# Optimization experiments

Hardware: AMD Instinct MI355X
Metric: run time of the kernel (lower is better)

## Reference

```python
import jax, jax.numpy as jnp
import numpy as np

H = 32        # num heads
D = 80        # head dim
HID = 2560    # hidden size = H*D
ROT = 32      # rotary dim = int(0.4*80)
THETA = 10000.0
T = 2048      # total packed tokens
B = 4         # sequences
SEQ = 512     # tokens per sequence
CACHE = 4096  # paged cache slots


def setup_inputs() -> dict:
    key = jax.random.key(0)
    ks = jax.random.split(key, 10)
    bound = 1.0 / np.sqrt(HID)

    def lin(k):
        kw, kb = jax.random.split(k)
        W = jax.random.uniform(kw, (HID, HID), jnp.float32, -bound, bound)
        b = jax.random.uniform(kb, (HID,), jnp.float32, -bound, bound)
        return W, b

    Wq, bq = lin(ks[0])
    Wk, bk = lin(ks[1])
    Wv, bv = lin(ks[2])
    Wd, bd = lin(ks[3])
    h = jax.random.normal(ks[4], (T, HID), jnp.float32)
    return {
        "h": h,
        "k_cache": jnp.zeros((CACHE, HID), jnp.float32),
        "v_cache": jnp.zeros((CACHE, HID), jnp.float32),
        "positions": (jnp.arange(T) % SEQ).astype(jnp.int32),
        "offsets": (jnp.arange(B + 1) * SEQ).astype(jnp.int32),
        "cache_indices": jnp.arange(T, dtype=jnp.int32),
        "Wq": Wq, "bq": bq, "Wk": Wk, "bk": bk,
        "Wv": Wv, "bv": bv, "Wd": Wd, "bd": bd,
    }


def _rotate_half(x):
    x1, x2 = jnp.split(x, 2, axis=-1)
    return jnp.concatenate([-x2, x1], axis=-1)


def reference(h, k_cache, v_cache, positions, offsets, cache_indices,
              Wq, bq, Wk, bk, Wv, bv, Wd, bd):
    # QKV projections (torch Linear: x @ W.T + b)
    q = h @ Wq.T + bq
    k = h @ Wk.T + bk
    v = h @ Wv.T + bv

    q3 = q.reshape(T, H, D)
    k3 = k.reshape(T, H, D)

    # partial RoPE on first ROT dims of each head
    pos = positions.astype(jnp.float32)
    inv_freq = 1.0 / (THETA ** (jnp.arange(0, ROT, 2, dtype=jnp.float32) / ROT))
    freqs = pos[:, None] * inv_freq                      # [T, ROT/2]
    emb = jnp.concatenate([freqs, freqs], axis=-1)       # [T, ROT]
    cos = jnp.cos(emb)[:, None, :]                       # [T, 1, ROT]
    sin = jnp.sin(emb)[:, None, :]

    q_rot, q_pass = q3[..., :ROT], q3[..., ROT:]
    k_rot, k_pass = k3[..., :ROT], k3[..., ROT:]
    q_rot = q_rot * cos + _rotate_half(q_rot) * sin
    k_rot = k_rot * cos + _rotate_half(k_rot) * sin
    q3 = jnp.concatenate([q_rot, q_pass], axis=-1)
    k3 = jnp.concatenate([k_rot, k_pass], axis=-1)

    # prompt_init=True path: scatter rotated k and v into paged caches
    new_k_cache = k_cache.at[cache_indices].set(k3.reshape(T, HID))
    new_v_cache = v_cache.at[cache_indices].set(v)

    # variable-length causal attention over packed sequences
    scale = D ** -0.5
    scores = jnp.einsum('thd,shd->hts', q3, k3) * scale   # [H, T, T]
    idx = jnp.arange(T)
    seg = jnp.searchsorted(offsets[1:], idx, side='right')
    mask = (seg[:, None] == seg[None, :]) & (idx[:, None] >= idx[None, :])
    scores = jnp.where(mask[None], scores, jnp.float32(-1e30))
    p = jax.nn.softmax(scores, axis=-1)
    o = jnp.einsum('hts,shd->thd', p, v.reshape(T, H, D)).reshape(T, HID)

    out = o @ Wd.T + bd
    return out, new_k_cache, new_v_cache
```

## Files before the change

### kernel.cpp

```cpp
#include <hip/hip_runtime.h>
#include <cstdint>
#include <cstddef>


#define HIDDEN 2560
#define SEQT 2048
#define NHEADS 32
#define DHEAD 80
#define NSEG 4
#define SEGLEN 512
#define CACHE_ROWS 4096
#define QSCALE 0.11180339887498949f

typedef __bf16 bf16_8 __attribute__((ext_vector_type(8)));
typedef unsigned short u16x8 __attribute__((ext_vector_type(8)));
typedef float f32x4 __attribute__((ext_vector_type(4)));

__device__ __forceinline__ unsigned short f2bf(float f) {
  unsigned int u = __builtin_bit_cast(unsigned int, f);
  u += 0x7fffu + ((u >> 16) & 1u);
  return (unsigned short)(u >> 16);
}
__device__ __forceinline__ float bf2f(unsigned short s) {
  unsigned int u = ((unsigned int)s) << 16;
  return __builtin_bit_cast(float, u);
}

__device__ __forceinline__ void gload16(const unsigned short* g, unsigned short* l) {
  __builtin_amdgcn_global_load_lds(
      (const __attribute__((address_space(1))) unsigned int*)g,
      (__attribute__((address_space(3))) unsigned int*)l, 16, 0, 0);
}

#define BAR() asm volatile("s_barrier" ::: "memory")
#define LGKM0()                                          \
  do {                                                   \
    asm volatile("s_waitcnt lgkmcnt(0)" ::: "memory");   \
    __builtin_amdgcn_sched_barrier(0);                   \
  } while (0)
#define PRIO(x) __builtin_amdgcn_s_setprio(x)
#define MF(af, bf, c) c = __builtin_amdgcn_mfma_f32_16x16x32_bf16(af, bf, c, 0, 0, 0)

__global__ __launch_bounds__(256) void cast5_kernel(
    const float* __restrict__ s0, const float* __restrict__ s1,
    const float* __restrict__ s2, const float* __restrict__ s3,
    const float* __restrict__ s4,
    unsigned short* __restrict__ d0, unsigned short* __restrict__ d1,
    unsigned short* __restrict__ d2, unsigned short* __restrict__ d3,
    unsigned short* __restrict__ d4) {
  const int z = blockIdx.z;
  const float* s = z == 0 ? s0 : z == 1 ? s1 : z == 2 ? s2 : z == 3 ? s3 : s4;
  unsigned short* d = z == 0 ? d0 : z == 1 ? d1 : z == 2 ? d2 : z == 3 ? d3 : d4;
  const int n4 = (z < 4) ? (HIDDEN * HIDDEN / 4) : (SEQT * HIDDEN / 4);
  int i = blockIdx.x * blockDim.x + threadIdx.x;
  const int stride = gridDim.x * blockDim.x;
  for (; i < n4; i += stride) {
    float4 v = ((const float4*)s)[i];
    ushort4 o;
    o.x = f2bf(v.x); o.y = f2bf(v.y); o.z = f2bf(v.z); o.w = f2bf(v.w);
    ((ushort4*)d)[i] = o;
  }
}

__global__ __launch_bounds__(256) void copy_upper_kernel(
    const float* __restrict__ kci, const float* __restrict__ vci,
    float* __restrict__ kco, float* __restrict__ vco) {
  const int n4half = SEQT * HIDDEN / 4;
  int i = blockIdx.x * blockDim.x + threadIdx.x;
  const int stride = gridDim.x * blockDim.x;
  for (; i < 2 * n4half; i += stride) {
    const int w = i >= n4half;
    const int j = i - w * n4half + n4half;
    const float4* s = w ? (const float4*)vci : (const float4*)kci;
    float4* d = w ? (float4*)vco : (float4*)kco;
    d[j] = s[j];
  }
}

template <int OUTMODE>
__device__ __forceinline__ void gemm256_body(
    const unsigned short* __restrict__ A, const unsigned short* __restrict__ Bg,
    const float* __restrict__ bias, void* __restrict__ C,
    int m0, int n0, int kbase, int nt) {
  constexpr int K = HIDDEN;
  __shared__ __align__(16) unsigned short L[65536];

  const int tid = threadIdx.x;
  const int lane = tid & 63;
  const int wid = tid >> 6;
  const int l15 = lane & 15;
  const int kg = lane >> 4;
  const int wm = wid >> 2;
  const int wn = wid & 3;

  const int g8 = (((tid & 7) - (tid >> 3)) & 7) * 8;
  const int srow = tid >> 3;
  const unsigned short* As0 = A + (size_t)(m0 + srow) * K + kbase + g8;
  const unsigned short* As1 = As0 + (size_t)128 * K;
  const unsigned short* Bs0 = Bg + (size_t)(n0 + srow) * K + kbase + g8;
  const unsigned short* Bs1 = Bs0 + (size_t)128 * K;
  const int t16 = tid * 8;

  auto stA0 = [&](int kt) {
    const int b = (kt & 1) * 32768, ko = kt * 64;
    gload16(As0 + ko, L + b + t16);
    gload16(As1 + ko, L + b + 8192 + t16);
  };
  auto stA1 = [&](int kt) {
    const int b = (kt & 1) * 32768, ko = 64 * K + kt * 64;
    gload16(As0 + ko, L + b + 4096 + t16);
    gload16(As1 + ko, L + b + 12288 + t16);
  };
  auto stB0 = [&](int kt) {
    const int b = (kt & 1) * 32768 + 16384, ko = kt * 64;
    gload16(Bs0 + ko, L + b + t16);
    gload16(Bs0 + 64 * K + ko, L + b + 4096 + t16);
  };
  auto stB1 = [&](int kt) {
    const int b = (kt & 1) * 32768 + 16384 + 8192, ko = kt * 64;
    gload16(Bs1 + ko, L + b + t16);
    gload16(Bs1 + 64 * K + ko, L + b + 4096 + t16);
  };

  const int c0 = (kg + l15) & 7;
  const int aof0 = wm * 8192 + l15 * 64 + c0 * 8;
  const int aof1 = wm * 8192 + l15 * 64 + (c0 ^ 4) * 8;
  const int bof0 = 16384 + wn * 4096 + l15 * 64 + c0 * 8;
  const int bof1 = 16384 + wn * 4096 + l15 * 64 + (c0 ^ 4) * 8;

  f32x4 acc[8][4];
#pragma unroll
  for (int m = 0; m < 8; m++)
#pragma unroll
    for (int n = 0; n < 4; n++) acc[m][n] = f32x4{0.f, 0.f, 0.f, 0.f};

  bf16_8 a[4][2], bl[2][2], bh[2][2];

#define DSR(off) (*(const bf16_8*)(L + (off)))
  auto rdA = [&](int off) {
#pragma unroll
    for (int fm = 0; fm < 4; fm++) {
      a[fm][0] = DSR(off + aof0 + fm * 1024);
      a[fm][1] = DSR(off + aof1 + fm * 1024);
    }
  };
  auto rdBl = [&](int off) {
#pragma unroll
    for (int fn = 0; fn < 2; fn++) {
      bl[fn][0] = DSR(off + bof0 + fn * 1024);
      bl[fn][1] = DSR(off + bof1 + fn * 1024);
    }
  };
  auto rdBh = [&](int off) {
#pragma unroll
    for (int fn = 0; fn < 2; fn++) {
      bh[fn][0] = DSR(off + bof0 + (2 + fn) * 1024);
      bh[fn][1] = DSR(off + bof1 + (2 + fn) * 1024);
    }
  };
  auto mmq = [&](int mq, int nq, bf16_8 (&bb)[2][2]) {
#pragma unroll
    for (int fm = 0; fm < 4; fm++)
#pragma unroll
      for (int fn = 0; fn < 2; fn++) {
        MF(a[fm][0], bb[fn][0], acc[mq * 4 + fm][nq * 2 + fn]);
        MF(a[fm][1], bb[fn][1], acc[mq * 4 + fm][nq * 2 + fn]);
      }
  };

  stA0(0); stB0(0); stB1(0); stA1(0);
  stA0(1); stB0(1); stB1(1);
  asm volatile("s_waitcnt vmcnt(6)" ::: "memory");
  BAR();

#pragma unroll 2
  for (int t = 0; t < nt - 2; ++t) {
    const int bo = (t & 1) * 32768;
    rdA(bo); rdBl(bo);
    stA1(t + 1);
    BAR(); LGKM0(); PRIO(1); mmq(0, 0, bl); PRIO(0); BAR();
    rdBh(bo);
    stA0(t + 2);
    BAR(); LGKM0(); PRIO(1); mmq(0, 1, bh); PRIO(0); BAR();
    rdA(bo + 4096);
    stB0(t + 2);
    BAR(); LGKM0(); PRIO(1); mmq(1, 0, bl); PRIO(0); BAR();
    stB1(t + 2);
    BAR(); PRIO(1); mmq(1, 1, bh); PRIO(0);
    asm volatile("s_waitcnt vmcnt(6)" ::: "memory");
    BAR();
  }

  {
    const int bo = 0;
    rdA(bo); rdBl(bo);
    stA1(nt - 1);
    BAR(); LGKM0(); PRIO(1); mmq(0, 0, bl); PRIO(0); BAR();
    rdBh(bo);
    BAR(); LGKM0(); PRIO(1); mmq(0, 1, bh); PRIO(0); BAR();
    rdA(bo + 4096);
    BAR(); LGKM0(); PRIO(1); mmq(1, 0, bl); PRIO(0); BAR();
    BAR(); PRIO(1); mmq(1, 1, bh); PRIO(0);
    asm volatile("s_waitcnt vmcnt(0)" ::: "memory");
    BAR();
  }
  {
    const int bo = 32768;
    rdA(bo); rdBl(bo);
    BAR(); LGKM0(); PRIO(1); mmq(0, 0, bl); PRIO(0); BAR();
    rdBh(bo);
    BAR(); LGKM0(); PRIO(1); mmq(0, 1, bh); PRIO(0); BAR();
    rdA(bo + 4096);
    BAR(); LGKM0(); PRIO(1); mmq(1, 0, bl); PRIO(0); BAR();
    PRIO(1); mmq(1, 1, bh); PRIO(0);
  }
#undef DSR

#pragma unroll
  for (int n4 = 0; n4 < 4; n4++) {
    const int col = n0 + wn * 64 + n4 * 16 + l15;
    const float bv = (OUTMODE == 2) ? 0.f : bias[col];
#pragma unroll
    for (int m8 = 0; m8 < 8; m8++) {
      const int rowb = m0 + wm * 128 + m8 * 16 + kg * 4;
#pragma unroll
      for (int j = 0; j < 4; j++) {
        float val = acc[m8][n4][j] + bv;
        if (OUTMODE == 0)
          ((unsigned short*)C)[(size_t)(rowb + j) * HIDDEN + col] = f2bf(val);
        else
          ((float*)C)[(size_t)(rowb + j) * HIDDEN + col] = val;
      }
    }
  }
}

__global__ __launch_bounds__(512, 2) void gemm_qkv8_kernel(
    const unsigned short* __restrict__ A,
    const unsigned short* __restrict__ B0, const unsigned short* __restrict__ B1,
    const unsigned short* __restrict__ B2,
    const float* __restrict__ bias0, const float* __restrict__ bias1,
    const float* __restrict__ bias2,
    unsigned short* __restrict__ C0, unsigned short* __restrict__ C1,
    unsigned short* __restrict__ C2) {
  const int lb = blockIdx.x + 8 * (blockIdx.y + 10 * blockIdx.z);
  const int swz = (lb & 7) * 30 + (lb >> 3);
  const int mx = swz & 7;
  const int r = swz >> 3;
  const int ny = r % 10;
  const int zz = r / 10;
  const unsigned short* B = zz == 0 ? B0 : (zz == 1 ? B1 : B2);
  const float* bias = zz == 0 ? bias0 : (zz == 1 ? bias1 : bias2);
  unsigned short* C = zz == 0 ? C0 : (zz == 1 ? C1 : C2);
  gemm256_body<0>(A, B, bias, C, mx * 256, ny * 256, 0, 40);
}

__global__ __launch_bounds__(512, 2) void gemm_out8_kernel(
    const unsigned short* __restrict__ A, const unsigned short* __restrict__ B,
    float* __restrict__ P0, float* __restrict__ P1, float* __restrict__ P2) {
  const int lb = blockIdx.x + 8 * (blockIdx.y + 10 * blockIdx.z);
  const int swz = (lb & 7) * 30 + (lb >> 3);
  const int mx = swz & 7;
  const int r = swz >> 3;
  const int ny = r % 10;
  const int kz = r / 10;
  float* P = kz == 0 ? P0 : (kz == 1 ? P1 : P2);
  const int kbase = kz * 896;
  const int nt = (kz == 2) ? 12 : 14;
  gemm256_body<2>(A, B, nullptr, P, mx * 256, ny * 256, kbase, nt);
}

__global__ __launch_bounds__(256) void reduce3_bias_kernel(
    const float* __restrict__ p0, const float* __restrict__ p1,
    const float* __restrict__ p2, const float* __restrict__ bias,
    float* __restrict__ out, int n4) {
  int i = blockIdx.x * blockDim.x + threadIdx.x;
  const int stride = gridDim.x * blockDim.x;
  for (; i < n4; i += stride) {
    float4 a = ((const float4*)p0)[i];
    float4 b = ((const float4*)p1)[i];
    float4 c = ((const float4*)p2)[i];
    const int cb = (i * 4) % HIDDEN;
    float4 bv = *(const float4*)&bias[cb];
    float4 o;
    o.x = a.x + b.x + c.x + bv.x;
    o.y = a.y + b.y + c.y + bv.y;
    o.z = a.z + b.z + c.z + bv.z;
    o.w = a.w + b.w + c.w + bv.w;
    ((float4*)out)[i] = o;
  }
}

__global__ __launch_bounds__(256) void rope_scatter_kernel(
    unsigned short* __restrict__ qb, unsigned short* __restrict__ kb,
    const unsigned short* __restrict__ vb,
    const int* __restrict__ positions, const int* __restrict__ cidx,
    float* __restrict__ kco, float* __restrict__ vco) {
  const int t = blockIdx.x;
  const int tid = threadIdx.x;
  __shared__ float cs[16], sn[16];

  if (tid < 16) {
    const float pos = (float)positions[t];
    const float inv = expf(-(float)tid * (9.210340371976184f / 16.0f));
    const float f = pos * inv;
    cs[tid] = cosf(f);
    sn[tid] = sinf(f);
  }
  __syncthreads();

  for (int i = tid; i < 1024; i += 256) {
    const int which = i >> 9;
    const int p = i & 511;
    const int hh = p >> 4, d = p & 15;
    unsigned short* buf = which ? kb : qb;
    const size_t base = (size_t)t * HIDDEN + hh * DHEAD + d;
    const float x1 = bf2f(buf[base]);
    const float x2 = bf2f(buf[base + 16]);
    const float c = cs[d], s = sn[d];
    buf[base] = f2bf(x1 * c - x2 * s);
    buf[base + 16] = f2bf(x2 * c + x1 * s);
  }
  __syncthreads();

  const int ci = cidx[t];
  float* krow = kco + (size_t)ci * HIDDEN;
  float* vrow = vco + (size_t)ci * HIDDEN;
  const unsigned short* ks = kb + (size_t)t * HIDDEN;
  const unsigned short* vs = vb + (size_t)t * HIDDEN;
  for (int i = tid; i < HIDDEN; i += 256) {
    krow[i] = bf2f(ks[i]);
    vrow[i] = bf2f(vs[i]);
  }
}

#define KSTR 104
#define VSTR 72
#define PSTR 72

__global__ __launch_bounds__(256) void attn_mfma_kernel(
    const unsigned short* __restrict__ qb, const unsigned short* __restrict__ kb,
    const unsigned short* __restrict__ vb, unsigned short* __restrict__ ob) {
  const int qt = blockIdx.x;
  const int h = blockIdx.y;
  const int seg = blockIdx.z;
  const int tq0 = seg * SEGLEN + qt * 64;

  __shared__ unsigned short Kt[64 * KSTR];
  __shared__ unsigned short VtT[80 * VSTR];
  __shared__ unsigned short Pw[4][16 * PSTR];

  const int tid = threadIdx.x;
  const int lane = tid & 63;
  const int w = tid >> 6;
  const int l15 = lane & 15;
  const int g = lane >> 4;

  bf16_8 qa[3];
  {
    const unsigned short* qp = qb + (size_t)(tq0 + w * 16 + l15) * HIDDEN + h * DHEAD;
#pragma unroll
    for (int c = 0; c < 3; c++) {
      u16x8 t = (u16x8)(unsigned short)0;
      const int d0 = c * 32 + g * 8;
      if (d0 < DHEAD) {
#pragma unroll
        for (int e = 0; e < 8; e++) t[e] = f2bf(bf2f(qp[d0 + e]) * QSCALE);
      }
      qa[c] = __builtin_bit_cast(bf16_8, t);
    }
  }

  float m_[4], l_[4];
#pragma unroll
  for (int j = 0; j < 4; j++) { m_[j] = -3.0e38f; l_[j] = 0.f; }
  f32x4 Oacc[5];
#pragma unroll
  for (int n = 0; n < 5; n++) Oacc[n] = f32x4{0.f, 0.f, 0.f, 0.f};

  for (int st = 0; st <= qt; ++st) {
    const int ts0 = seg * SEGLEN + st * 64;
    __syncthreads();
    for (int i = tid; i < 64 * 20; i += 256) {
      const int row = i / 20;
      const int c = i - row * 20;
      const size_t gsrc = (size_t)(ts0 + row) * HIDDEN + h * DHEAD + c * 4;
      ushort4 kv = *(const ushort4*)(kb + gsrc);
      ushort4 vv = *(const ushort4*)(vb + gsrc);
      *(ushort4*)&Kt[row * KSTR + c * 4] = kv;
      VtT[(c * 4 + 0) * VSTR + row] = vv.x;
      VtT[(c * 4 + 1) * VSTR + row] = vv.y;
      VtT[(c * 4 + 2) * VSTR + row] = vv.z;
      VtT[(c * 4 + 3) * VSTR + row] = vv.w;
    }
    __syncthreads();

    f32x4 Sacc[4];
#pragma unroll
    for (int t = 0; t < 4; t++) Sacc[t] = f32x4{0.f, 0.f, 0.f, 0.f};
#pragma unroll
    for (int c = 0; c < 3; c++) {
#pragma unroll
      for (int t = 0; t < 4; t++) {
        bf16_8 kf;
        if (c < 2 || g < 2)
          kf = *(const bf16_8*)&Kt[(t * 16 + l15) * KSTR + c * 32 + g * 8];
        else
          kf = __builtin_bit_cast(bf16_8, (u16x8)(unsigned short)0);
        Sacc[t] = __builtin_amdgcn_mfma_f32_16x16x32_bf16(qa[c], kf, Sacc[t], 0, 0, 0);
      }
    }

    if (st == qt) {
#pragma unroll
      for (int t = 0; t < 4; t++)
#pragma unroll
        for (int j = 0; j < 4; j++)
          if (t * 16 + l15 > w * 16 + 4 * g + j) Sacc[t][j] = -1e30f;
    }

    float pm[4], ps[4], rold[4];
#pragma unroll
    for (int j = 0; j < 4; j++)
      pm[j] = fmaxf(fmaxf(Sacc[0][j], Sacc[1][j]), fmaxf(Sacc[2][j], Sacc[3][j]));
#pragma unroll
    for (int d = 1; d < 16; d <<= 1)
#pragma unroll
      for (int j = 0; j < 4; j++) pm[j] = fmaxf(pm[j], __shfl_xor(pm[j], d, 64));
#pragma unroll
    for (int j = 0; j < 4; j++) {
      const float mn = fmaxf(m_[j], pm[j]);
      rold[j] = __expf(m_[j] - mn);
      m_[j] = mn;
      ps[j] = 0.f;
    }
#pragma unroll
    for (int t = 0; t < 4; t++)
#pragma unroll
      for (int j = 0; j < 4; j++) {
        const float p = __expf(Sacc[t][j] - m_[j]);
        Sacc[t][j] = p;
        ps[j] += p;
      }
#pragma unroll
    for (int d = 1; d < 16; d <<= 1)
#pragma unroll
      for (int j = 0; j < 4; j++) ps[j] += __shfl_xor(ps[j], d, 64);
#pragma unroll
    for (int j = 0; j < 4; j++) l_[j] = l_[j] * rold[j] + ps[j];

#pragma unroll
    for (int t = 0; t < 4; t++)
#pragma unroll
      for (int j = 0; j < 4; j++)
        Pw[w][(4 * g + j) * PSTR + t * 16 + l15] = f2bf(Sacc[t][j]);
#pragma unroll
    for (int n = 0; n < 5; n++)
#pragma unroll
      for (int j = 0; j < 4; j++) Oacc[n][j] *= rold[j];

#pragma unroll
    for (int c = 0; c < 2; c++) {
      bf16_8 pa = *(const bf16_8*)&Pw[w][l15 * PSTR + c * 32 + g * 8];
#pragma unroll
      for (int n = 0; n < 5; n++) {
        bf16_8 vf = *(const bf16_8*)&VtT[(n * 16 + l15) * VSTR + c * 32 + g * 8];
        Oacc[n] = __builtin_amdgcn_mfma_f32_16x16x32_bf16(pa, vf, Oacc[n], 0, 0, 0);
      }
    }
  }

  float inv[4];
#pragma unroll
  for (int j = 0; j < 4; j++) inv[j] = 1.f / l_[j];
  unsigned short* op = ob + (size_t)(tq0 + w * 16) * HIDDEN + h * DHEAD;
#pragma unroll
  for (int n = 0; n < 5; n++)
#pragma unroll
    for (int j = 0; j < 4; j++)
      op[(size_t)(4 * g + j) * HIDDEN + n * 16 + l15] = f2bf(Oacc[n][j] * inv[j]);
}

extern "C" void kernel_launch(void* const* d_in, const int* in_sizes, int n_in,
                              void* d_out, int out_size, void* d_ws, size_t ws_size,
                              hipStream_t stream) {
  const float* h = (const float*)d_in[0];
  const float* kci = (const float*)d_in[1];
  const float* vci = (const float*)d_in[2];
  const int* positions = (const int*)d_in[3];
  const int* cidx = (const int*)d_in[5];
  const float* Wq = (const float*)d_in[6];
  const float* bq = (const float*)d_in[7];
  const float* Wk = (const float*)d_in[8];
  const float* bk = (const float*)d_in[9];
  const float* Wv = (const float*)d_in[10];
  const float* bv = (const float*)d_in[11];
  const float* Wd = (const float*)d_in[12];
  const float* bd = (const float*)d_in[13];

  float* out = (float*)d_out;
  float* kco = out + (size_t)SEQT * HIDDEN;
  float* vco = kco + (size_t)CACHE_ROWS * HIDDEN;

  char* ws = (char*)d_ws;
  char* ws0 = ws;
  unsigned short* h_bf = (unsigned short*)ws;  ws += (size_t)SEQT * HIDDEN * 2;
  unsigned short* Wq_bf = (unsigned short*)ws; ws += (size_t)HIDDEN * HIDDEN * 2;
  unsigned short* Wk_bf = (unsigned short*)ws; ws += (size_t)HIDDEN * HIDDEN * 2;
  unsigned short* Wv_bf = (unsigned short*)ws; ws += (size_t)HIDDEN * HIDDEN * 2;
  unsigned short* Wd_bf = (unsigned short*)ws; ws += (size_t)HIDDEN * HIDDEN * 2;
  unsigned short* q_bf = (unsigned short*)ws;  ws += (size_t)SEQT * HIDDEN * 2;
  unsigned short* k_bf = (unsigned short*)ws;  ws += (size_t)SEQT * HIDDEN * 2;
  unsigned short* v_bf = (unsigned short*)ws;  ws += (size_t)SEQT * HIDDEN * 2;
  unsigned short* o_bf = (unsigned short*)ws;  ws += (size_t)SEQT * HIDDEN * 2;

  float* part0 = (float*)ws0;
  float* part1 = part0 + (size_t)SEQT * HIDDEN;
  float* part2 = (float*)q_bf;

  copy_upper_kernel<<<2048, 256, 0, stream>>>(kci, vci, kco, vco);

  {
    dim3 gc(2048, 1, 5);
    cast5_kernel<<<gc, 256, 0, stream>>>(Wq, Wk, Wv, Wd, h,
                                         Wq_bf, Wk_bf, Wv_bf, Wd_bf, h_bf);
  }

  {
    dim3 gq(SEQT / 256, HIDDEN / 256, 3);
    gemm_qkv8_kernel<<<gq, 512, 0, stream>>>(h_bf, Wq_bf, Wk_bf, Wv_bf, bq, bk, bv,
                                             q_bf, k_bf, v_bf);
  }

  rope_scatter_kernel<<<SEQT, 256, 0, stream>>>(q_bf, k_bf, v_bf, positions, cidx, kco, vco);

  {
    dim3 ga(SEGLEN / 64, NHEADS, NSEG);
    attn_mfma_kernel<<<ga, 256, 0, stream>>>(q_bf, k_bf, v_bf, o_bf);
  }

  {
    dim3 go(SEQT / 256, HIDDEN / 256, 3);
    gemm_out8_kernel<<<go, 512, 0, stream>>>(o_bf, Wd_bf, part0, part1, part2);
  }
  reduce3_bias_kernel<<<2048, 256, 0, stream>>>(part0, part1, part2, bd, out,
                                                SEQT * HIDDEN / 4);
}
```

Measured before the change: 249.9 us.

## Use 32x32x16 MFMA in GEMM body and merge cast and cache-copy kernels

The shared GEMM body switches from 16x16x32 to 32x32x16 bf16 MFMA tiles. LDS read offsets are rebuilt with a new swizzle, and the accumulator layout and epilogue row mapping change to match. The larger instruction is meant to cut LDS fragment reads per flop and raise MFMA throughput. Separately, the weight/activation cast and the upper-cache copy are folded into one launch with a 7-deep z grid, saving a kernel launch and letting the two run concurrently. The risk is that the new LDS access pattern causes bank conflicts and that the epilogue stores become less coalesced.

New measurement: 259.6 us. +3.9%, slower.

```diff
diff --git a/kernel.cpp b/kernel.cpp
--- a/kernel.cpp
+++ b/kernel.cpp
@@ -15,6 +15,7 @@
 typedef __bf16 bf16_8 __attribute__((ext_vector_type(8)));
 typedef unsigned short u16x8 __attribute__((ext_vector_type(8)));
 typedef float f32x4 __attribute__((ext_vector_type(4)));
+typedef float f32x16 __attribute__((ext_vector_type(16)));
 
 __device__ __forceinline__ unsigned short f2bf(float f) {
   unsigned int u = __builtin_bit_cast(unsigned int, f);
@@ -39,41 +40,34 @@
     __builtin_amdgcn_sched_barrier(0);                   \
   } while (0)
 #define PRIO(x) __builtin_amdgcn_s_setprio(x)
-#define MF(af, bf, c) c = __builtin_amdgcn_mfma_f32_16x16x32_bf16(af, bf, c, 0, 0, 0)
-
-__global__ __launch_bounds__(256) void cast5_kernel(
+
+__global__ __launch_bounds__(256) void prep_kernel(
     const float* __restrict__ s0, const float* __restrict__ s1,
     const float* __restrict__ s2, const float* __restrict__ s3,
     const float* __restrict__ s4,
+    const float* __restrict__ kci, const float* __restrict__ vci,
     unsigned short* __restrict__ d0, unsigned short* __restrict__ d1,
     unsigned short* __restrict__ d2, unsigned short* __restrict__ d3,
-    unsigned short* __restrict__ d4) {
+    unsigned short* __restrict__ d4,
+    float* __restrict__ kco, float* __restrict__ vco) {
   const int z = blockIdx.z;
-  const float* s = z == 0 ? s0 : z == 1 ? s1 : z == 2 ? s2 : z == 3 ? s3 : s4;
-  unsigned short* d = z == 0 ? d0 : z == 1 ? d1 : z == 2 ? d2 : z == 3 ? d3 : d4;
-  const int n4 = (z < 4) ? (HIDDEN * HIDDEN / 4) : (SEQT * HIDDEN / 4);
+  const int stride = gridDim.x * blockDim.x;
   int i = blockIdx.x * blockDim.x + threadIdx.x;
-  const int stride = gridDim.x * blockDim.x;
-  for (; i < n4; i += stride) {
-    float4 v = ((const float4*)s)[i];
-    ushort4 o;
-    o.x = f2bf(v.x); o.y = f2bf(v.y); o.z = f2bf(v.z); o.w = f2bf(v.w);
-    ((ushort4*)d)[i] = o;
-  }
-}
-
-__global__ __launch_bounds__(256) void copy_upper_kernel(
-    const float* __restrict__ kci, const float* __restrict__ vci,
-    float* __restrict__ kco, float* __restrict__ vco) {
-  const int n4half = SEQT * HIDDEN / 4;
-  int i = blockIdx.x * blockDim.x + threadIdx.x;
-  const int stride = gridDim.x * blockDim.x;
-  for (; i < 2 * n4half; i += stride) {
-    const int w = i >= n4half;
-    const int j = i - w * n4half + n4half;
-    const float4* s = w ? (const float4*)vci : (const float4*)kci;
-    float4* d = w ? (float4*)vco : (float4*)kco;
-    d[j] = s[j];
+  if (z < 5) {
+    const float* s = z == 0 ? s0 : z == 1 ? s1 : z == 2 ? s2 : z == 3 ? s3 : s4;
+    unsigned short* d = z == 0 ? d0 : z == 1 ? d1 : z == 2 ? d2 : z == 3 ? d3 : d4;
+    const int n4 = (z < 4) ? (HIDDEN * HIDDEN / 4) : (SEQT * HIDDEN / 4);
+    for (; i < n4; i += stride) {
+      float4 v = ((const float4*)s)[i];
+      ushort4 o;
+      o.x = f2bf(v.x); o.y = f2bf(v.y); o.z = f2bf(v.z); o.w = f2bf(v.w);
+      ((ushort4*)d)[i] = o;
+    }
+  } else {
+    const int n4 = SEQT * HIDDEN / 4;
+    const float4* s = (const float4*)(z == 5 ? kci : vci);
+    float4* d = (float4*)(z == 5 ? kco : vco);
+    for (; i < n4; i += stride) d[i + n4] = s[i + n4];
   }
 }
 
@@ -88,8 +82,8 @@
   const int tid = threadIdx.x;
   const int lane = tid & 63;
   const int wid = tid >> 6;
-  const int l15 = lane & 15;
-  const int kg = lane >> 4;
+  const int l31 = lane & 31;
+  const int l5 = lane >> 5;
   const int wm = wid >> 2;
   const int wn = wid & 3;
 
@@ -122,50 +116,38 @@
     gload16(Bs1 + 64 * K + ko, L + b + 4096 + t16);
   };
 
-  const int c0 = (kg + l15) & 7;
-  const int aof0 = wm * 8192 + l15 * 64 + c0 * 8;
-  const int aof1 = wm * 8192 + l15 * 64 + (c0 ^ 4) * 8;
-  const int bof0 = 16384 + wn * 4096 + l15 * 64 + c0 * 8;
-  const int bof1 = 16384 + wn * 4096 + l15 * 64 + (c0 ^ 4) * 8;
-
-  f32x4 acc[8][4];
-#pragma unroll
-  for (int m = 0; m < 8; m++)
-#pragma unroll
-    for (int n = 0; n < 4; n++) acc[m][n] = f32x4{0.f, 0.f, 0.f, 0.f};
-
-  bf16_8 a[4][2], bl[2][2], bh[2][2];
+  int cslot[4];
+#pragma unroll
+  for (int ks = 0; ks < 4; ks++) cslot[ks] = ((l31 + l5 + 2 * ks) & 7) * 8;
+
+  f32x16 acc[4][2];
+#pragma unroll
+  for (int m = 0; m < 4; m++)
+#pragma unroll
+    for (int n = 0; n < 2; n++) acc[m][n] = (f32x16)(0.f);
+
+  bf16_8 a[2][4], b0[4], b1[4];
 
 #define DSR(off) (*(const bf16_8*)(L + (off)))
-  auto rdA = [&](int off) {
-#pragma unroll
-    for (int fm = 0; fm < 4; fm++) {
-      a[fm][0] = DSR(off + aof0 + fm * 1024);
-      a[fm][1] = DSR(off + aof1 + fm * 1024);
-    }
-  };
-  auto rdBl = [&](int off) {
-#pragma unroll
-    for (int fn = 0; fn < 2; fn++) {
-      bl[fn][0] = DSR(off + bof0 + fn * 1024);
-      bl[fn][1] = DSR(off + bof1 + fn * 1024);
-    }
-  };
-  auto rdBh = [&](int off) {
-#pragma unroll
-    for (int fn = 0; fn < 2; fn++) {
-      bh[fn][0] = DSR(off + bof0 + (2 + fn) * 1024);
-      bh[fn][1] = DSR(off + bof1 + (2 + fn) * 1024);
-    }
-  };
-  auto mmq = [&](int mq, int nq, bf16_8 (&bb)[2][2]) {
-#pragma unroll
-    for (int fm = 0; fm < 4; fm++)
-#pragma unroll
-      for (int fn = 0; fn < 2; fn++) {
-        MF(a[fm][0], bb[fn][0], acc[mq * 4 + fm][nq * 2 + fn]);
-        MF(a[fm][1], bb[fn][1], acc[mq * 4 + fm][nq * 2 + fn]);
-      }
+  auto rdA = [&](int off, int mq) {
+#pragma unroll
+    for (int f = 0; f < 2; f++)
+#pragma unroll
+      for (int ks = 0; ks < 4; ks++)
+        a[f][ks] = DSR(off + wm * 8192 + (mq * 2 + f) * 2048 + l31 * 64 + cslot[ks]);
+  };
+  auto rdB = [&](int off, int fn, bf16_8 (&bb)[4]) {
+#pragma unroll
+    for (int ks = 0; ks < 4; ks++)
+      bb[ks] = DSR(off + 16384 + wn * 4096 + fn * 2048 + l31 * 64 + cslot[ks]);
+  };
+  auto mm = [&](int mq, int nq, bf16_8 (&bb)[4]) {
+#pragma unroll
+    for (int f = 0; f < 2; f++)
+#pragma unroll
+      for (int ks = 0; ks < 4; ks++)
+        acc[mq * 2 + f][nq] = __builtin_amdgcn_mfma_f32_32x32x16_bf16(
+            a[f][ks], bb[ks], acc[mq * 2 + f][nq], 0, 0, 0);
   };
 
   stA0(0); stB0(0); stB1(0); stA1(0);
@@ -176,60 +158,61 @@
 #pragma unroll 2
   for (int t = 0; t < nt - 2; ++t) {
     const int bo = (t & 1) * 32768;
-    rdA(bo); rdBl(bo);
+    rdA(bo, 0); rdB(bo, 0, b0);
     stA1(t + 1);
-    BAR(); LGKM0(); PRIO(1); mmq(0, 0, bl); PRIO(0); BAR();
-    rdBh(bo);
+    BAR(); LGKM0(); PRIO(1); mm(0, 0, b0); PRIO(0); BAR();
+    rdB(bo, 1, b1);
     stA0(t + 2);
-    BAR(); LGKM0(); PRIO(1); mmq(0, 1, bh); PRIO(0); BAR();
-    rdA(bo + 4096);
+    BAR(); LGKM0(); PRIO(1); mm(0, 1, b1); PRIO(0); BAR();
+    rdA(bo, 1);
     stB0(t + 2);
-    BAR(); LGKM0(); PRIO(1); mmq(1, 0, bl); PRIO(0); BAR();
+    BAR(); LGKM0(); PRIO(1); mm(1, 0, b0); PRIO(0); BAR();
     stB1(t + 2);
-    BAR(); PRIO(1); mmq(1, 1, bh); PRIO(0);
+    BAR(); PRIO(1); mm(1, 1, b1); PRIO(0);
     asm volatile("s_waitcnt vmcnt(6)" ::: "memory");
     BAR();
   }
 
   {
     const int bo = 0;
-    rdA(bo); rdBl(bo);
+    rdA(bo, 0); rdB(bo, 0, b0);
     stA1(nt - 1);
-    BAR(); LGKM0(); PRIO(1); mmq(0, 0, bl); PRIO(0); BAR();
-    rdBh(bo);
-    BAR(); LGKM0(); PRIO(1); mmq(0, 1, bh); PRIO(0); BAR();
-    rdA(bo + 4096);
-    BAR(); LGKM0(); PRIO(1); mmq(1, 0, bl); PRIO(0); BAR();
-    BAR(); PRIO(1); mmq(1, 1, bh); PRIO(0);
+    BAR(); LGKM0(); PRIO(1); mm(0, 0, b0); PRIO(0); BAR();
+    rdB(bo, 1, b1);
+    BAR(); LGKM0(); PRIO(1); mm(0, 1, b1); PRIO(0); BAR();
+    rdA(bo, 1);
+    BAR(); LGKM0(); PRIO(1); mm(1, 0, b0); PRIO(0); BAR();
+    BAR(); PRIO(1); mm(1, 1, b1); PRIO(0);
     asm volatile("s_waitcnt vmcnt(0)" ::: "memory");
     BAR();
   }
   {
     const int bo = 32768;
-    rdA(bo); rdBl(bo);
-    BAR(); LGKM0(); PRIO(1); mmq(0, 0, bl); PRIO(0); BAR();
-    rdBh(bo);
-    BAR(); LGKM0(); PRIO(1); mmq(0, 1, bh); PRIO(0); BAR();
-    rdA(bo + 4096);
-    BAR(); LGKM0(); PRIO(1); mmq(1, 0, bl); PRIO(0); BAR();
-    PRIO(1); mmq(1, 1, bh); PRIO(0);
+    rdA(bo, 0); rdB(bo, 0, b0);
+    BAR(); LGKM0(); PRIO(1); mm(0, 0, b0); PRIO(0); BAR();
+    rdB(bo, 1, b1);
+    BAR(); LGKM0(); PRIO(1); mm(0, 1, b1); PRIO(0); BAR();
+    rdA(bo, 1);
+    BAR(); LGKM0(); PRIO(1); mm(1, 0, b0); PRIO(0); BAR();
+    PRIO(1); mm(1, 1, b1); PRIO(0);
   }
 #undef DSR
 
 #pragma unroll
-  for (int n4 = 0; n4 < 4; n4++) {
-    const int col = n0 + wn * 64 + n4 * 16 + l15;
+  for (int fn = 0; fn < 2; fn++) {
+    const int col = n0 + wn * 64 + fn * 32 + l31;
     const float bv = (OUTMODE == 2) ? 0.f : bias[col];
 #pragma unroll
-    for (int m8 = 0; m8 < 8; m8++) {
-      const int rowb = m0 + wm * 128 + m8 * 16 + kg * 4;
-#pragma unroll
-      for (int j = 0; j < 4; j++) {
-        float val = acc[m8][n4][j] + bv;
+    for (int fm = 0; fm < 4; fm++) {
+      const int rowb = m0 + wm * 128 + fm * 32 + 4 * l5;
+#pragma unroll
+      for (int reg = 0; reg < 16; reg++) {
+        const int row = rowb + (reg & 3) + 8 * (reg >> 2);
+        float val = acc[fm][fn][reg] + bv;
         if (OUTMODE == 0)
-          ((unsigned short*)C)[(size_t)(rowb + j) * HIDDEN + col] = f2bf(val);
+          ((unsigned short*)C)[(size_t)row * HIDDEN + col] = f2bf(val);
         else
-          ((float*)C)[(size_t)(rowb + j) * HIDDEN + col] = val;
+          ((float*)C)[(size_t)row * HIDDEN + col] = val;
       }
     }
   }
@@ -518,12 +501,11 @@
   float* part1 = part0 + (size_t)SEQT * HIDDEN;
   float* part2 = (float*)q_bf;
 
-  copy_upper_kernel<<<2048, 256, 0, stream>>>(kci, vci, kco, vco);
-
-  {
-    dim3 gc(2048, 1, 5);
-    cast5_kernel<<<gc, 256, 0, stream>>>(Wq, Wk, Wv, Wd, h,
-                                         Wq_bf, Wk_bf, Wv_bf, Wd_bf, h_bf);
+  {
+    dim3 gp(2048, 1, 7);
+    prep_kernel<<<gp, 256, 0, stream>>>(Wq, Wk, Wv, Wd, h, kci, vci,
+                                        Wq_bf, Wk_bf, Wv_bf, Wd_bf, h_bf,
+                                        kco, vco);
   }
 
   {
```
